# Kernel optimization log

Hardware: AMD Instinct MI355X
Metric: run time of the kernel (lower is better)

## Reference

```python
import jax, jax.numpy as jnp
import numpy as np

B, H, D, DV, N, M = 1, 8, 64, 64, 2048, 128


def setup_inputs() -> dict:
    key = jax.random.key(0)
    k1, k2, k3, k4 = jax.random.split(key, 4)
    keys = jax.random.normal(k1, (B, H, D, N), dtype=jnp.float32)
    values = jax.random.normal(k2, (B, H, DV, N), dtype=jnp.float32)
    queries = jax.random.normal(k3, (B, H, D, N), dtype=jnp.float32)
    # orthonormal random features: QR of (m, key_dim) gaussian (reduced QR, m >= key_dim)
    raw = np.asarray(jax.random.normal(k4, (M, D), dtype=jnp.float32), dtype=np.float64)
    features = jnp.asarray(np.linalg.qr(raw)[0], dtype=jnp.float32)  # (M, D)
    return {"keys": keys, "values": values, "queries": queries, "features": features}


def reference(keys, values, queries, features):
    b, h, d, n = keys.shape
    dv = values.shape[2]
    m = features.shape[0]
    phi_scale = 1.0 / jnp.sqrt(jnp.asarray(m, keys.dtype))
    # flatten heads into batch, move locations to axis 1: (B*H, N, D)
    k = keys.reshape(b * h, d, n).transpose(0, 2, 1)
    v = values.reshape(b * h, dv, n).transpose(0, 2, 1)
    q = queries.reshape(b * h, d, n).transpose(0, 2, 1)

    def phi(x):  # (BH, N, D) -> (BH, N, M); f=[relu], h(x)=1.0
        return jax.nn.relu(jnp.einsum('bnd,md->bnm', x, features)) * phi_scale

    phi_k = phi(k)
    phi_q = phi(q)
    # causal linear attention: prefix sums of phi_k (x) v outer products
    kv = jnp.cumsum(phi_k[:, :, :, None] * v[:, :, None, :], axis=1)  # (BH, N, M, DV)
    out = jnp.einsum('bnm,bnmv->bnv', phi_q, kv)                      # (BH, N, DV)
    norm = jnp.einsum('bnm,bnm->bn', phi_q, jnp.cumsum(phi_k, axis=1))
    out = out / norm[:, :, None]
    out = out.transpose(0, 2, 1).reshape(b, h, dv, n)
    return out
```

## Files before the change

kernel.cpp:

```cpp
#include <hip/hip_runtime.h>


#define BH 8
#define D 64
#define DV 64
#define NSEQ 2048
#define M 128
#define CHK 64
#define NC (NSEQ / CHK)
#define PHI_SCALE 0.08838834764831845f

typedef unsigned int uint;
typedef unsigned short ushort;
typedef __attribute__((ext_vector_type(8))) short bf16x8;
typedef __attribute__((ext_vector_type(4))) short bf16x4;
typedef __attribute__((ext_vector_type(4))) float f32x4;
#define MFMA16(a, b, c) __builtin_amdgcn_mfma_f32_16x16x32_bf16((a), (b), (c), 0, 0, 0)

__device__ __forceinline__ short f2bf(float x) {
    uint u = __float_as_uint(x);
    u += 0x7fffu + ((u >> 16) & 1u);
    return (short)(u >> 16);
}
__device__ __forceinline__ float bf2f(short b) {
    return __uint_as_float(((uint)(ushort)b) << 16);
}

#define SWZ64(r, c)  ((r) * 64  + ((c) ^ (((r) & 7) << 3)))
#define SWZ128(r, c) ((r) * 128 + ((c) ^ (((r) & 7) << 3)))

__global__ __launch_bounds__(256, 2) void favor_p1(
    const float* __restrict__ keys, const float* __restrict__ values,
    const float* __restrict__ queries, const float* __restrict__ features,
    ushort* __restrict__ St, float* __restrict__ z,
    ushort* __restrict__ pQg, ushort* __restrict__ pKg)
{
    const int mh = blockIdx.x >> 8, cid = blockIdx.x & 255;
    const int bh = cid >> 5, c = cid & 31, n0 = c * CHK;
    const int tid = threadIdx.x;
    const int lane = tid & 63, wid = tid >> 6, quad = lane >> 4, l16 = lane & 15;

    __shared__ ulong2 smv[2048];
    short* sF    = (short*)smv;
    short* sPKmn = (short*)smv + 4096;
    short* sPQt  = (short*)smv + 8192;
    short* sPKt  = (short*)smv + 12288;

    for (int k = 0; k < 4; ++k) {
        const int i = tid + 256 * k;
        float4 f = ((const float4*)features)[mh * 1024 + i];
        const int e = 4 * i, row = e >> 6, col = e & 63;
        bf16x4 bq;
        bq[0] = f2bf(f.x); bq[1] = f2bf(f.y); bq[2] = f2bf(f.z); bq[3] = f2bf(f.w);
        *(bf16x4*)(sF + SWZ64(row, col)) = bq;
    }
    const float* Kb = keys    + bh * D * NSEQ + n0 + 16 * wid + l16;
    const float* Qb = queries + bh * D * NSEQ + n0 + 16 * wid + l16;
    bf16x8 bK[2], aQ[2], aV[2];
    for (int h = 0; h < 2; ++h)
        for (int j = 0; j < 8; ++j) {
            const int d = 32 * h + 8 * quad + j;
            bK[h][j] = f2bf(Kb[d * NSEQ]);
            aQ[h][j] = f2bf(Qb[d * NSEQ]);
        }
    {
        const float* Vb = values + bh * DV * NSEQ + n0;
        for (int h = 0; h < 2; ++h) {
            const float4* vp = (const float4*)(Vb + (16 * wid + l16) * NSEQ + 32 * h + 8 * quad);
            float4 v0 = vp[0], v1 = vp[1];
            aV[h][0] = f2bf(v0.x); aV[h][1] = f2bf(v0.y);
            aV[h][2] = f2bf(v0.z); aV[h][3] = f2bf(v0.w);
            aV[h][4] = f2bf(v1.x); aV[h][5] = f2bf(v1.y);
            aV[h][6] = f2bf(v1.z); aV[h][7] = f2bf(v1.w);
        }
    }
    __syncthreads();

    for (int mt = 0; mt < 4; ++mt) {
        f32x4 aMN = {0.f,0.f,0.f,0.f}, aQm = {0.f,0.f,0.f,0.f}, aKm = {0.f,0.f,0.f,0.f};
        for (int h = 0; h < 2; ++h) {
            bf16x8 fF = *(const bf16x8*)(sF + SWZ64(16 * mt + l16, 32 * h + 8 * quad));
            aMN = MFMA16(fF, bK[h], aMN);
            aQm = MFMA16(aQ[h], fF, aQm);
            aKm = MFMA16(bK[h], fF, aKm);
        }
        for (int r = 0; r < 4; ++r) {
            const int mr = 16 * mt + 4 * quad + r;
            sPKmn[SWZ64(mr, 16 * wid + l16)] = f2bf(fmaxf(aMN[r], 0.f) * PHI_SCALE);
            const int nr = 16 * wid + 4 * quad + r;
            sPQt[SWZ64(nr, 16 * mt + l16)] = f2bf(fmaxf(aQm[r], 0.f) * PHI_SCALE);
            sPKt[SWZ64(nr, 16 * mt + l16)] = f2bf(fmaxf(aKm[r], 0.f) * PHI_SCALE);
        }
    }
    __syncthreads();

    if (tid < 64) {
        float s = 0.f;
        for (int n = 0; n < 64; ++n) s += bf2f(sPKmn[SWZ64(tid, (n + tid) & 63)]);
        z[(bh * NC + c) * M + mh * 64 + tid] = s;
    }

    {
        ushort* So = St + (size_t)(bh * NC + c) * (DV * M);
        for (int mt = 0; mt < 4; ++mt) {
            f32x4 acc = {0.f,0.f,0.f,0.f};
            for (int h = 0; h < 2; ++h) {
                bf16x8 bP = *(const bf16x8*)(sPKmn + SWZ64(16 * mt + l16, 32 * h + 8 * quad));
                acc = MFMA16(aV[h], bP, acc);
            }
            for (int r = 0; r < 4; ++r)
                So[(16 * wid + 4 * quad + r) * M + mh * 64 + 16 * mt + l16] =
                    (ushort)f2bf(acc[r]);
        }
    }

    {
        ushort* pQc = pQg + (size_t)(bh * NC + c) * 8192;
        ushort* pKc = pKg + (size_t)(bh * NC + c) * 8192;
        const ulong2* sq = (const ulong2*)sPQt;
        const ulong2* sk = (const ulong2*)sPKt;
        for (int i = tid; i < 512; i += 256) {
            const int row = i >> 3, q = i & 7;
            ((ulong2*)pQc)[row * 16 + mh * 8 + q] = sq[i];
            ((ulong2*)pKc)[row * 16 + mh * 8 + q] = sk[i];
        }
    }
}

__global__ __launch_bounds__(256, 2) void favor_p2(ushort* __restrict__ St,
                                                   float* __restrict__ z)
{
    __shared__ float carry[128];
    const int tid = threadIdx.x;
    if (blockIdx.x < 512) {
        const int col = blockIdx.x * 128 + (tid & 127);
        const int half = tid >> 7;
        const int bh = col >> 13, vm = col & 8191;
        ushort* p = St + (size_t)bh * NC * 8192 + vm;
        float vals[16];
        #pragma unroll
        for (int k = 0; k < 16; ++k) vals[k] = bf2f(p[(16 * half + k) * 8192]);
        if (half == 0) {
            float total = 0.f;
            #pragma unroll
            for (int k = 0; k < 16; ++k) total += vals[k];
            carry[tid] = total;
        }
        __syncthreads();
        float run = (half == 0) ? 0.f : carry[tid & 127];
        #pragma unroll
        for (int k = 0; k < 16; ++k) {
            p[(16 * half + k) * 8192] = (ushort)f2bf(run);
            run += vals[k];
        }
    } else {
        const int i = (blockIdx.x - 512) * 256 + tid;
        const int bh = i >> 7, m = i & 127;
        float* p = z + bh * NC * M + m;
        float vals[NC];
        #pragma unroll
        for (int cc = 0; cc < NC; ++cc) vals[cc] = p[cc * M];
        float run = 0.f;
        #pragma unroll
        for (int cc = 0; cc < NC; ++cc) { p[cc * M] = run; run += vals[cc]; }
    }
}

__global__ __launch_bounds__(256, 2) void favor_p3(
    const float* __restrict__ values, const ushort* __restrict__ St,
    const float* __restrict__ z, const ushort* __restrict__ pQg,
    const ushort* __restrict__ pKg, float* __restrict__ out)
{
    const int vh = blockIdx.x >> 8, cid = blockIdx.x & 255;
    const int bh = cid >> 5, c = cid & 31, n0 = c * CHK;
    const int tid = threadIdx.x;
    const int lane = tid & 63, wid = tid >> 6, quad = lane >> 4, l16 = lane & 15;

    __shared__ ulong2 smv[2928];
    short* sPQt = (short*)smv;
    short* sPKt = (short*)smv + 8192;
    short* sV   = (short*)smv + 16384;
    short* sAm  = (short*)smv + 18432;
    float* sNm  = (float*)((char*)smv + 45056);
    float* sNmP = (float*)((char*)smv + 45312);
    float* sZ   = (float*)((char*)smv + 46336);
    float* sOut = (float*)smv;

    const ushort* Sb = St + (size_t)(bh * NC + c) * (DV * M);
    bf16x8 bS[4][2];
    #pragma unroll
    for (int mt = 0; mt < 4; ++mt)
        #pragma unroll
        for (int vt = 0; vt < 2; ++vt)
            bS[mt][vt] = *(const bf16x8*)(Sb + (vh * 32 + 16 * vt + l16) * M
                                             + 32 * mt + 8 * quad);

    {
        const ulong2* pQc = (const ulong2*)(pQg + (size_t)(bh * NC + c) * 8192);
        const ulong2* pKc = (const ulong2*)(pKg + (size_t)(bh * NC + c) * 8192);
        ulong2* dq = (ulong2*)sPQt;
        ulong2* dk = (ulong2*)sPKt;
        for (int i = tid; i < 1024; i += 256) {
            dq[i] = pQc[i];
            dk[i] = pKc[i];
        }
    }
    {
        const int vrow = tid >> 3, cb = (tid & 7) * 8;
        const float4* vp = (const float4*)(values + (bh * DV + vh * 32 + vrow) * NSEQ
                                                  + n0 + cb);
        float4 f0 = vp[0], f1 = vp[1];
        bf16x8 w;
        w[0] = f2bf(f0.x); w[1] = f2bf(f0.y); w[2] = f2bf(f0.z); w[3] = f2bf(f0.w);
        w[4] = f2bf(f1.x); w[5] = f2bf(f1.y); w[6] = f2bf(f1.z); w[7] = f2bf(f1.w);
        *(bf16x8*)(sV + SWZ64(vrow, cb)) = w;
    }
    if (tid < 128) sZ[tid] = z[(bh * NC + c) * M + tid];
    __syncthreads();

    f32x4 accO[2], accC[4];
    accO[0] = (f32x4){0.f,0.f,0.f,0.f}; accO[1] = (f32x4){0.f,0.f,0.f,0.f};
    for (int t = 0; t < 4; ++t) accC[t] = (f32x4){0.f,0.f,0.f,0.f};
    for (int mt = 0; mt < 4; ++mt) {
        bf16x8 aP = *(const bf16x8*)(sPQt + SWZ128(16 * wid + l16, 32 * mt + 8 * quad));
        for (int jt = 0; jt < 4; ++jt) {
            bf16x8 bK2 = *(const bf16x8*)(sPKt + SWZ128(16 * jt + l16, 32 * mt + 8 * quad));
            accC[jt] = MFMA16(aP, bK2, accC[jt]);
        }
    }
    float rsum[4] = {0.f, 0.f, 0.f, 0.f};
    for (int jt = 0; jt < 4; ++jt)
        for (int r = 0; r < 4; ++r) {
            const int n = 16 * wid + 4 * quad + r;
            const int j = 16 * jt + l16;
            const float av = (j <= n) ? accC[jt][r] : 0.f;
            rsum[r] += av;
            sAm[SWZ64(n, j)] = f2bf(av);
        }
    for (int r = 0; r < 4; ++r) {
        float s = rsum[r];
        s += __shfl_xor(s, 1); s += __shfl_xor(s, 2);
        s += __shfl_xor(s, 4); s += __shfl_xor(s, 8);
        if (l16 == 0) sNm[16 * wid + 4 * quad + r] = s;
    }

    for (int mt = 0; mt < 4; ++mt) {
        bf16x8 aP = *(const bf16x8*)(sPQt + SWZ128(16 * wid + l16, 32 * mt + 8 * quad));
        for (int vt = 0; vt < 2; ++vt)
            accO[vt] = MFMA16(aP, bS[mt][vt], accO[vt]);
    }
    {
        const int n = tid & 63, g = tid >> 6;
        float s = 0.f;
        for (int mm = 0; mm < 32; ++mm) {
            const int m = 32 * g + ((mm + n) & 31);
            s += bf2f(sPQt[SWZ128(n, m)]) * sZ[m];
        }
        sNmP[n * 4 + g] = s;
    }
    __syncthreads();

    for (int jh = 0; jh < 2; ++jh) {
        bf16x8 aA = *(const bf16x8*)(sAm + SWZ64(16 * wid + l16, 32 * jh + 8 * quad));
        for (int vt = 0; vt < 2; ++vt) {
            bf16x8 bV = *(const bf16x8*)(sV + SWZ64(16 * vt + l16, 32 * jh + 8 * quad));
            accO[vt] = MFMA16(aA, bV, accO[vt]);
        }
    }
    if (tid < 64)
        sNm[tid] += sNmP[tid * 4] + sNmP[tid * 4 + 1] + sNmP[tid * 4 + 2] + sNmP[tid * 4 + 3];
    __syncthreads();

    for (int vt = 0; vt < 2; ++vt)
        for (int r = 0; r < 4; ++r) {
            const int n = 16 * wid + 4 * quad + r, vl = 16 * vt + l16;
            sOut[n * 33 + vl] = accO[vt][r] / sNm[n];
        }
    __syncthreads();
    for (int i = tid; i < 2048; i += 256) {
        const int vl = i >> 6, n = i & 63;
        out[(bh * DV + vh * 32 + vl) * NSEQ + n0 + n] = sOut[n * 33 + vl];
    }
}

extern "C" void kernel_launch(void* const* d_in, const int* in_sizes, int n_in,
                              void* d_out, int out_size, void* d_ws, size_t ws_size,
                              hipStream_t stream)
{
    (void)in_sizes; (void)n_in; (void)out_size; (void)ws_size;
    const float* keys     = (const float*)d_in[0];
    const float* values   = (const float*)d_in[1];
    const float* queries  = (const float*)d_in[2];
    const float* features = (const float*)d_in[3];
    float* outp = (float*)d_out;

    char* w = (char*)d_ws;
    ushort* St  = (ushort*)w;
    float*  z   = (float*)(w + (size_t)4 * 1024 * 1024);
    ushort* pQg = (ushort*)(w + (size_t)4 * 1024 * 1024 + 128 * 1024);
    ushort* pKg = (ushort*)(w + (size_t)8 * 1024 * 1024 + 128 * 1024);

    favor_p1<<<dim3(512), dim3(256), 0, stream>>>(keys, values, queries, features,
                                                  St, z, pQg, pKg);
    favor_p2<<<dim3(516), dim3(256), 0, stream>>>(St, z);
    favor_p3<<<dim3(512), dim3(256), 0, stream>>>(values, St, z, pQg, pKg, outp);
}
```

Baseline: 88.49 us.

## Fuse three FAVOR phases into one kernel with inter-block flag synchronization

Merges the chunk-state, prefix-scan and output kernels into a single kernel. Blocks publish per-chunk states and wait on atomic flags for all earlier chunks, then each block sums the preceding chunk states itself instead of relying on a separate scan kernel. This removes two kernel launches and the scan pass, but adds a spin-wait that depends on all 512 blocks being co-resident, plus redundant O(c) prefix summation per block and a memset launch.

After: 198.9 us. 125% more time.

```diff
diff --git a/kernel.cpp b/kernel.cpp
--- a/kernel.cpp
+++ b/kernel.cpp
@@ -29,26 +29,39 @@
 #define SWZ64(r, c)  ((r) * 64  + ((c) ^ (((r) & 7) << 3)))
 #define SWZ128(r, c) ((r) * 128 + ((c) ^ (((r) & 7) << 3)))
 
-__global__ __launch_bounds__(256, 2) void favor_p1(
+__global__ __launch_bounds__(256, 2) void favor_one(
     const float* __restrict__ keys, const float* __restrict__ values,
     const float* __restrict__ queries, const float* __restrict__ features,
     ushort* __restrict__ St, float* __restrict__ z,
-    ushort* __restrict__ pQg, ushort* __restrict__ pKg)
+    ushort* __restrict__ pQg, ushort* __restrict__ pKg,
+    int* __restrict__ flags, float* __restrict__ out)
 {
-    const int mh = blockIdx.x >> 8, cid = blockIdx.x & 255;
+    const int hb = blockIdx.x >> 8, cid = blockIdx.x & 255;
     const int bh = cid >> 5, c = cid & 31, n0 = c * CHK;
     const int tid = threadIdx.x;
     const int lane = tid & 63, wid = tid >> 6, quad = lane >> 4, l16 = lane & 15;
 
-    __shared__ ulong2 smv[2048];
-    short* sF    = (short*)smv;
-    short* sPKmn = (short*)smv + 4096;
-    short* sPQt  = (short*)smv + 8192;
-    short* sPKt  = (short*)smv + 12288;
+    __shared__ ulong2 smv[3440];
+    char* sm = (char*)smv;
+    short* sF    = (short*)sm;
+    short* sPKmn = (short*)(sm + 8192);
+    short* sPQtH = (short*)(sm + 16384);
+    short* sPKtH = (short*)(sm + 24576);
+    short* sV    = (short*)(sm + 32768);
+    short* sPQ0  = (short*)sm;
+    short* sPQ1  = (short*)(sm + 8192);
+    short* sPK0  = (short*)(sm + 16384);
+    short* sPK1  = (short*)(sm + 24576);
+    short* sSx   = (short*)(sm + 36864);
+    short* sAm   = (short*)(sm + 45056);
+    float* sNm   = (float*)(sm + 53248);
+    float* sNmP  = (float*)(sm + 53504);
+    float* sZ    = (float*)(sm + 54528);
+    float* sOut  = (float*)sm;
 
     for (int k = 0; k < 4; ++k) {
         const int i = tid + 256 * k;
-        float4 f = ((const float4*)features)[mh * 1024 + i];
+        float4 f = ((const float4*)features)[hb * 1024 + i];
         const int e = 4 * i, row = e >> 6, col = e & 63;
         bf16x4 bq;
         bq[0] = f2bf(f.x); bq[1] = f2bf(f.y); bq[2] = f2bf(f.z); bq[3] = f2bf(f.w);
@@ -74,6 +87,16 @@
             aV[h][6] = f2bf(v1.z); aV[h][7] = f2bf(v1.w);
         }
     }
+    {
+        const int vrow = tid >> 3, cb2 = (tid & 7) * 8;
+        const float4* vp = (const float4*)(values + (bh * DV + hb * 32 + vrow) * NSEQ
+                                                  + n0 + cb2);
+        float4 f0 = vp[0], f1 = vp[1];
+        bf16x8 wv;
+        wv[0] = f2bf(f0.x); wv[1] = f2bf(f0.y); wv[2] = f2bf(f0.z); wv[3] = f2bf(f0.w);
+        wv[4] = f2bf(f1.x); wv[5] = f2bf(f1.y); wv[6] = f2bf(f1.z); wv[7] = f2bf(f1.w);
+        *(bf16x8*)(sV + SWZ64(vrow, cb2)) = wv;
+    }
     __syncthreads();
 
     for (int mt = 0; mt < 4; ++mt) {
@@ -88,8 +111,8 @@
             const int mr = 16 * mt + 4 * quad + r;
             sPKmn[SWZ64(mr, 16 * wid + l16)] = f2bf(fmaxf(aMN[r], 0.f) * PHI_SCALE);
             const int nr = 16 * wid + 4 * quad + r;
-            sPQt[SWZ64(nr, 16 * mt + l16)] = f2bf(fmaxf(aQm[r], 0.f) * PHI_SCALE);
-            sPKt[SWZ64(nr, 16 * mt + l16)] = f2bf(fmaxf(aKm[r], 0.f) * PHI_SCALE);
+            sPQtH[SWZ64(nr, 16 * mt + l16)] = f2bf(fmaxf(aQm[r], 0.f) * PHI_SCALE);
+            sPKtH[SWZ64(nr, 16 * mt + l16)] = f2bf(fmaxf(aKm[r], 0.f) * PHI_SCALE);
         }
     }
     __syncthreads();
@@ -97,9 +120,8 @@
     if (tid < 64) {
         float s = 0.f;
         for (int n = 0; n < 64; ++n) s += bf2f(sPKmn[SWZ64(tid, (n + tid) & 63)]);
-        z[(bh * NC + c) * M + mh * 64 + tid] = s;
-    }
-
+        z[(bh * NC + c) * M + hb * 64 + tid] = s;
+    }
     {
         ushort* So = St + (size_t)(bh * NC + c) * (DV * M);
         for (int mt = 0; mt < 4; ++mt) {
@@ -109,122 +131,80 @@
                 acc = MFMA16(aV[h], bP, acc);
             }
             for (int r = 0; r < 4; ++r)
-                So[(16 * wid + 4 * quad + r) * M + mh * 64 + 16 * mt + l16] =
+                So[(16 * wid + 4 * quad + r) * M + hb * 64 + 16 * mt + l16] =
                     (ushort)f2bf(acc[r]);
         }
     }
-
     {
         ushort* pQc = pQg + (size_t)(bh * NC + c) * 8192;
         ushort* pKc = pKg + (size_t)(bh * NC + c) * 8192;
-        const ulong2* sq = (const ulong2*)sPQt;
-        const ulong2* sk = (const ulong2*)sPKt;
+        const ulong2* sq = (const ulong2*)sPQtH;
+        const ulong2* sk = (const ulong2*)sPKtH;
         for (int i = tid; i < 512; i += 256) {
             const int row = i >> 3, q = i & 7;
-            ((ulong2*)pQc)[row * 16 + mh * 8 + q] = sq[i];
-            ((ulong2*)pKc)[row * 16 + mh * 8 + q] = sk[i];
-        }
-    }
-}
-
-__global__ __launch_bounds__(256, 2) void favor_p2(ushort* __restrict__ St,
-                                                   float* __restrict__ z)
-{
-    __shared__ float carry[128];
-    const int tid = threadIdx.x;
-    if (blockIdx.x < 512) {
-        const int col = blockIdx.x * 128 + (tid & 127);
-        const int half = tid >> 7;
-        const int bh = col >> 13, vm = col & 8191;
-        ushort* p = St + (size_t)bh * NC * 8192 + vm;
-        float vals[16];
-        #pragma unroll
-        for (int k = 0; k < 16; ++k) vals[k] = bf2f(p[(16 * half + k) * 8192]);
-        if (half == 0) {
-            float total = 0.f;
-            #pragma unroll
-            for (int k = 0; k < 16; ++k) total += vals[k];
-            carry[tid] = total;
-        }
-        __syncthreads();
-        float run = (half == 0) ? 0.f : carry[tid & 127];
-        #pragma unroll
-        for (int k = 0; k < 16; ++k) {
-            p[(16 * half + k) * 8192] = (ushort)f2bf(run);
-            run += vals[k];
-        }
-    } else {
-        const int i = (blockIdx.x - 512) * 256 + tid;
-        const int bh = i >> 7, m = i & 127;
-        float* p = z + bh * NC * M + m;
-        float vals[NC];
-        #pragma unroll
-        for (int cc = 0; cc < NC; ++cc) vals[cc] = p[cc * M];
-        float run = 0.f;
-        #pragma unroll
-        for (int cc = 0; cc < NC; ++cc) { p[cc * M] = run; run += vals[cc]; }
-    }
-}
-
-__global__ __launch_bounds__(256, 2) void favor_p3(
-    const float* __restrict__ values, const ushort* __restrict__ St,
-    const float* __restrict__ z, const ushort* __restrict__ pQg,
-    const ushort* __restrict__ pKg, float* __restrict__ out)
-{
-    const int vh = blockIdx.x >> 8, cid = blockIdx.x & 255;
-    const int bh = cid >> 5, c = cid & 31, n0 = c * CHK;
-    const int tid = threadIdx.x;
-    const int lane = tid & 63, wid = tid >> 6, quad = lane >> 4, l16 = lane & 15;
-
-    __shared__ ulong2 smv[2928];
-    short* sPQt = (short*)smv;
-    short* sPKt = (short*)smv + 8192;
-    short* sV   = (short*)smv + 16384;
-    short* sAm  = (short*)smv + 18432;
-    float* sNm  = (float*)((char*)smv + 45056);
-    float* sNmP = (float*)((char*)smv + 45312);
-    float* sZ   = (float*)((char*)smv + 46336);
-    float* sOut = (float*)smv;
-
-    const ushort* Sb = St + (size_t)(bh * NC + c) * (DV * M);
-    bf16x8 bS[4][2];
-    #pragma unroll
-    for (int mt = 0; mt < 4; ++mt)
-        #pragma unroll
-        for (int vt = 0; vt < 2; ++vt)
-            bS[mt][vt] = *(const bf16x8*)(Sb + (vh * 32 + 16 * vt + l16) * M
-                                             + 32 * mt + 8 * quad);
+            ((ulong2*)pQc)[row * 16 + hb * 8 + q] = sq[i];
+            ((ulong2*)pKc)[row * 16 + hb * 8 + q] = sk[i];
+        }
+    }
+
+    __syncthreads();
+    __threadfence();
+    if (tid == 0)
+        __hip_atomic_fetch_add(&flags[bh * NC + c], 1,
+                               __ATOMIC_RELEASE, __HIP_MEMORY_SCOPE_AGENT);
+    for (int i = tid; i <= c; i += 256)
+        while (__hip_atomic_load(&flags[bh * NC + i],
+                                 __ATOMIC_ACQUIRE, __HIP_MEMORY_SCOPE_AGENT) < 2)
+            __builtin_amdgcn_s_sleep(2);
+    __syncthreads();
+    __threadfence();
 
     {
         const ulong2* pQc = (const ulong2*)(pQg + (size_t)(bh * NC + c) * 8192);
         const ulong2* pKc = (const ulong2*)(pKg + (size_t)(bh * NC + c) * 8192);
-        ulong2* dq = (ulong2*)sPQt;
-        ulong2* dk = (ulong2*)sPKt;
+        ulong2* dq = (ulong2*)sm;
+        ulong2* dk = (ulong2*)(sm + 16384);
         for (int i = tid; i < 1024; i += 256) {
-            dq[i] = pQc[i];
-            dk[i] = pKc[i];
-        }
-    }
-    {
-        const int vrow = tid >> 3, cb = (tid & 7) * 8;
-        const float4* vp = (const float4*)(values + (bh * DV + vh * 32 + vrow) * NSEQ
-                                                  + n0 + cb);
-        float4 f0 = vp[0], f1 = vp[1];
-        bf16x8 w;
-        w[0] = f2bf(f0.x); w[1] = f2bf(f0.y); w[2] = f2bf(f0.z); w[3] = f2bf(f0.w);
-        w[4] = f2bf(f1.x); w[5] = f2bf(f1.y); w[6] = f2bf(f1.z); w[7] = f2bf(f1.w);
-        *(bf16x8*)(sV + SWZ64(vrow, cb)) = w;
-    }
-    if (tid < 128) sZ[tid] = z[(bh * NC + c) * M + tid];
+            const int row = i >> 4, hh = (i >> 3) & 1, q = i & 7;
+            dq[hh * 512 + row * 8 + q] = pQc[i];
+            dk[hh * 512 + row * 8 + q] = pKc[i];
+        }
+    }
+    {
+        float a0[8] = {0.f,0.f,0.f,0.f,0.f,0.f,0.f,0.f};
+        float a1[8] = {0.f,0.f,0.f,0.f,0.f,0.f,0.f,0.f};
+        const ushort* Sb = St + (size_t)bh * NC * 8192 + hb * 4096 + 16 * tid;
+        for (int cc = 0; cc < c; ++cc) {
+            bf16x8 v0 = *(const bf16x8*)(Sb + (size_t)cc * 8192);
+            bf16x8 v1 = *(const bf16x8*)(Sb + (size_t)cc * 8192 + 8);
+            #pragma unroll
+            for (int j = 0; j < 8; ++j) { a0[j] += bf2f(v0[j]); a1[j] += bf2f(v1[j]); }
+        }
+        const int r = tid >> 3, cb = (16 * tid) & 127;
+        bf16x8 w0, w1;
+        #pragma unroll
+        for (int j = 0; j < 8; ++j) { w0[j] = f2bf(a0[j]); w1[j] = f2bf(a1[j]); }
+        *(bf16x8*)(sSx + SWZ128(r, cb))     = w0;
+        *(bf16x8*)(sSx + SWZ128(r, cb + 8)) = w1;
+    }
+    if (tid < 128) {
+        float s = 0.f;
+        const float* zp = z + bh * NC * M + tid;
+        for (int cc = 0; cc < c; ++cc) s += zp[cc * M];
+        sZ[tid] = s;
+    }
     __syncthreads();
 
     f32x4 accO[2], accC[4];
     accO[0] = (f32x4){0.f,0.f,0.f,0.f}; accO[1] = (f32x4){0.f,0.f,0.f,0.f};
     for (int t = 0; t < 4; ++t) accC[t] = (f32x4){0.f,0.f,0.f,0.f};
     for (int mt = 0; mt < 4; ++mt) {
-        bf16x8 aP = *(const bf16x8*)(sPQt + SWZ128(16 * wid + l16, 32 * mt + 8 * quad));
+        const short* qh = (mt < 2) ? sPQ0 : sPQ1;
+        const short* kh = (mt < 2) ? sPK0 : sPK1;
+        const int cb = 32 * (mt & 1) + 8 * quad;
+        bf16x8 aP = *(const bf16x8*)(qh + SWZ64(16 * wid + l16, cb));
         for (int jt = 0; jt < 4; ++jt) {
-            bf16x8 bK2 = *(const bf16x8*)(sPKt + SWZ128(16 * jt + l16, 32 * mt + 8 * quad));
+            bf16x8 bK2 = *(const bf16x8*)(kh + SWZ64(16 * jt + l16, cb));
             accC[jt] = MFMA16(aP, bK2, accC[jt]);
         }
     }
@@ -243,18 +223,22 @@
         s += __shfl_xor(s, 4); s += __shfl_xor(s, 8);
         if (l16 == 0) sNm[16 * wid + 4 * quad + r] = s;
     }
-
     for (int mt = 0; mt < 4; ++mt) {
-        bf16x8 aP = *(const bf16x8*)(sPQt + SWZ128(16 * wid + l16, 32 * mt + 8 * quad));
-        for (int vt = 0; vt < 2; ++vt)
-            accO[vt] = MFMA16(aP, bS[mt][vt], accO[vt]);
+        const short* qh = (mt < 2) ? sPQ0 : sPQ1;
+        const int cb = 32 * (mt & 1) + 8 * quad;
+        bf16x8 aP = *(const bf16x8*)(qh + SWZ64(16 * wid + l16, cb));
+        for (int vt = 0; vt < 2; ++vt) {
+            bf16x8 bS = *(const bf16x8*)(sSx + SWZ128(16 * vt + l16, 32 * mt + 8 * quad));
+            accO[vt] = MFMA16(aP, bS, accO[vt]);
+        }
     }
     {
         const int n = tid & 63, g = tid >> 6;
+        const short* qh = (g < 2) ? sPQ0 : sPQ1;
         float s = 0.f;
         for (int mm = 0; mm < 32; ++mm) {
             const int m = 32 * g + ((mm + n) & 31);
-            s += bf2f(sPQt[SWZ128(n, m)]) * sZ[m];
+            s += bf2f(qh[SWZ64(n, m & 63)]) * sZ[m];
         }
         sNmP[n * 4 + g] = s;
     }
@@ -279,7 +263,7 @@
     __syncthreads();
     for (int i = tid; i < 2048; i += 256) {
         const int vl = i >> 6, n = i & 63;
-        out[(bh * DV + vh * 32 + vl) * NSEQ + n0 + n] = sOut[n * 33 + vl];
+        out[(bh * DV + hb * 32 + vl) * NSEQ + n0 + n] = sOut[n * 33 + vl];
     }
 }
 
@@ -295,13 +279,13 @@
     float* outp = (float*)d_out;
 
     char* w = (char*)d_ws;
-    ushort* St  = (ushort*)w;
-    float*  z   = (float*)(w + (size_t)4 * 1024 * 1024);
-    ushort* pQg = (ushort*)(w + (size_t)4 * 1024 * 1024 + 128 * 1024);
-    ushort* pKg = (ushort*)(w + (size_t)8 * 1024 * 1024 + 128 * 1024);
-
-    favor_p1<<<dim3(512), dim3(256), 0, stream>>>(keys, values, queries, features,
-                                                  St, z, pQg, pKg);
-    favor_p2<<<dim3(516), dim3(256), 0, stream>>>(St, z);
-    favor_p3<<<dim3(512), dim3(256), 0, stream>>>(values, St, z, pQg, pKg, outp);
-}
+    ushort* St   = (ushort*)w;
+    float*  z    = (float*)(w + (size_t)4 * 1024 * 1024);
+    ushort* pQg  = (ushort*)(w + (size_t)4 * 1024 * 1024 + 128 * 1024);
+    ushort* pKg  = (ushort*)(w + (size_t)8 * 1024 * 1024 + 128 * 1024);
+    int*   flags = (int*)  (w + (size_t)12 * 1024 * 1024 + 128 * 1024);
+
+    hipMemsetAsync(flags, 0, BH * NC * sizeof(int), stream);
+    favor_one<<<dim3(512), dim3(256), 0, stream>>>(keys, values, queries, features,
+                                                   St, z, pQg, pKg, flags, outp);
+}
```
